# Optimization experiments

Measured on AMD Instinct MI355X. Metric: run time of the kernel, lower is better.

Reference implementation:

```python
import jax, jax.numpy as jnp
import numpy as np

K = 128
HEADS = 8
B = 4
T = 2048


def setup_inputs() -> dict:
    key = jax.random.key(0)
    ks = jax.random.split(key, 6)
    x = jax.random.normal(ks[0], (B, T, K), dtype=jnp.float32)
    s = 1.0 / np.sqrt(K)
    # torch nn.Linear weights are (out_features, in_features)
    Wq = jax.random.uniform(ks[1], (HEADS * K, K), dtype=jnp.float32, minval=-s, maxval=s)
    Wk = jax.random.uniform(ks[2], (HEADS * K, K), dtype=jnp.float32, minval=-s, maxval=s)
    Wv = jax.random.uniform(ks[3], (HEADS * K, K), dtype=jnp.float32, minval=-s, maxval=s)
    su = 1.0 / np.sqrt(HEADS * K)
    Wu = jax.random.uniform(ks[4], (K, HEADS * K), dtype=jnp.float32, minval=-su, maxval=su)
    bu = jax.random.uniform(ks[5], (K,), dtype=jnp.float32, minval=-su, maxval=su)
    return {"x": x, "Wq": Wq, "Wk": Wk, "Wv": Wv, "Wu": Wu, "bu": bu}


def reference(x, Wq, Wk, Wv, Wu, bu):
    b, t, k = x.shape
    h = HEADS
    # project: Linear(k, k*h) then view(b,t,h,k); weight reshaped to (h, k_out, k_in)
    q = jnp.einsum('btk,hdk->bhtd', x, Wq.reshape(h, k, k))
    kk = jnp.einsum('btk,hdk->bhtd', x, Wk.reshape(h, k, k))
    v = jnp.einsum('btk,hdk->bhtd', x, Wv.reshape(h, k, k))
    scale = jnp.asarray(k, x.dtype) ** 0.25
    q = q / scale
    kk = kk / scale
    dot = jnp.einsum('bhtd,bhsd->bhts', q, kk)  # [b,h,t,t]
    att = jax.nn.softmax(dot, axis=-1)
    out = jnp.einsum('bhts,bhsd->bhtd', att, v)  # [b,h,t,k]
    out = out.transpose(0, 2, 1, 3).reshape(b, t, h * k)
    return out @ Wu.T + bu
```

## Files before the change

kernel.cpp:

```cpp
#include <hip/hip_runtime.h>
#include <cmath>

namespace {

constexpr int HEADS = 8;
constexpr int Bn = 4;
constexpr int Tn = 2048;
constexpr int Dn = 128;
constexpr float Q_PRESCALE = 0.1275174340f;

typedef _Float16 half8 __attribute__((ext_vector_type(8)));
typedef _Float16 half4 __attribute__((ext_vector_type(4)));
typedef _Float16 half2v __attribute__((ext_vector_type(2)));
typedef float f32x4 __attribute__((ext_vector_type(4)));
typedef float f32x16 __attribute__((ext_vector_type(16)));
typedef unsigned int u32;
typedef unsigned int u32x4 __attribute__((ext_vector_type(4)));

__global__ __launch_bounds__(256) void cast_kernel(
    const float* __restrict__ x, const float* __restrict__ Wq, const float* __restrict__ Wk,
    const float* __restrict__ Wv, const float* __restrict__ Wu, _Float16* __restrict__ xh,
    _Float16* __restrict__ WH) {
  const int idx = blockIdx.x * 256 + threadIdx.x;
  const size_t base = (size_t)idx * 8;
  const float* src;
  _Float16* dst;
  if (base < 1048576) {
    src = x + base;
    dst = xh + base;
  } else {
    const size_t r = base - 1048576;
    const int s = (int)(r >> 17);
    src = ((s == 0) ? Wq : (s == 1) ? Wk : (s == 2) ? Wv : Wu) + (r & 131071);
    dst = WH + r;
  }
  const float4 a = *reinterpret_cast<const float4*>(src);
  const float4 b = *reinterpret_cast<const float4*>(src + 4);
  half8 h;
  h[0] = (_Float16)a.x; h[1] = (_Float16)a.y; h[2] = (_Float16)a.z; h[3] = (_Float16)a.w;
  h[4] = (_Float16)b.x; h[5] = (_Float16)b.y; h[6] = (_Float16)b.z; h[7] = (_Float16)b.w;
  *reinterpret_cast<half8*>(dst) = h;
}

__global__ __launch_bounds__(256, 4) void proj_kernel(const _Float16* __restrict__ xh,
                                                      const _Float16* __restrict__ WH,
                                                      _Float16* __restrict__ Qh,
                                                      _Float16* __restrict__ Kh,
                                                      _Float16* __restrict__ Vt) {
  __shared__ _Float16 sB[128 * 136];
  const int tid = threadIdx.x;
  const int w = tid >> 6, lane = tid & 63, quad = lane >> 4, l16 = lane & 15;
  const int m0 = blockIdx.x * 128;
  const int n0 = blockIdx.y * 128;

#pragma unroll
  for (int it = 0; it < 8; ++it) {
    const int fid = tid + it * 256;
    const int r = fid >> 4, g = fid & 15;
    const half8 v = *reinterpret_cast<const half8*>(WH + (size_t)(n0 + r) * 128 + g * 8);
    const int p = g ^ (r & 15);
    *reinterpret_cast<half8*>(sB + r * 128 + p * 8) = v;
  }

  half8 af[2][4];
  const _Float16* xp = xh + (size_t)(m0 + w * 32 + l16) * 128 + quad * 8;
#pragma unroll
  for (int mt = 0; mt < 2; ++mt)
#pragma unroll
    for (int kk = 0; kk < 4; ++kk)
      af[mt][kk] = *reinterpret_cast<const half8*>(xp + mt * 16 * 128 + kk * 32);

  __syncthreads();

  f32x4 acc[2][8];
#pragma unroll
  for (int mt = 0; mt < 2; ++mt)
#pragma unroll
    for (int nt = 0; nt < 8; ++nt) acc[mt][nt] = (f32x4){0.f, 0.f, 0.f, 0.f};

#pragma unroll
  for (int kk = 0; kk < 4; ++kk)
#pragma unroll
    for (int nt = 0; nt < 8; ++nt) {
      const int r = nt * 16 + l16;
      const int p = (kk * 4 + quad) ^ l16;
      const half8 bf = *reinterpret_cast<const half8*>(sB + r * 128 + p * 8);
      acc[0][nt] = __builtin_amdgcn_mfma_f32_16x16x32_f16(af[0][kk], bf, acc[0][nt], 0, 0, 0);
      acc[1][nt] = __builtin_amdgcn_mfma_f32_16x16x32_f16(af[1][kk], bf, acc[1][nt], 0, 0, 0);
    }

  const int sel = n0 >> 10;
  const int h = (n0 >> 7) & 7;
  const int b = m0 >> 11;
  const int t0b = m0 & 2047;
  const int bh = b * HEADS + h;
  const float scale = (sel == 0) ? Q_PRESCALE : 1.0f;

  __syncthreads();

  if (sel < 2) {
#pragma unroll
    for (int mt = 0; mt < 2; ++mt)
#pragma unroll
      for (int nt = 0; nt < 8; ++nt)
#pragma unroll
        for (int r = 0; r < 4; ++r)
          sB[(w * 32 + mt * 16 + quad * 4 + r) * 136 + nt * 16 + l16] =
              (_Float16)(acc[mt][nt][r] * scale);
  } else {
#pragma unroll
    for (int mt = 0; mt < 2; ++mt)
#pragma unroll
      for (int nt = 0; nt < 8; ++nt)
#pragma unroll
        for (int r = 0; r < 4; ++r)
          sB[(nt * 16 + l16) * 136 + w * 32 + mt * 16 + quad * 4 + r] = (_Float16)acc[mt][nt][r];
  }
  __syncthreads();

  _Float16* dstbase;
  size_t rstride;
  if (sel == 0) {
    dstbase = Qh + ((size_t)bh * Tn + t0b) * Dn;
    rstride = Dn;
  } else if (sel == 1) {
    dstbase = Kh + ((size_t)bh * Tn + t0b) * Dn;
    rstride = Dn;
  } else {
    dstbase = Vt + ((size_t)bh * Dn) * Tn + t0b;
    rstride = Tn;
  }
#pragma unroll
  for (int it = 0; it < 8; ++it) {
    const int fid = tid + it * 256;
    const int r = fid >> 4, g = fid & 15;
    const half8 v = *reinterpret_cast<const half8*>(sB + r * 136 + g * 8);
    *reinterpret_cast<half8*>(dstbase + (size_t)r * rstride + g * 8) = v;
  }
}

__global__ __launch_bounds__(512, 2) void flash_kernel(const _Float16* __restrict__ Qh,
                                                       const _Float16* __restrict__ Kh,
                                                       const _Float16* __restrict__ Vt,
                                                       _Float16* __restrict__ Obh) {
  __shared__ _Float16 sAll[40960];

  const int tid = threadIdx.x;
  const int w = tid >> 6;
  const int lane = tid & 63;
  const int l31 = lane & 31;
  const int h = lane >> 5;
  const int qt = blockIdx.x;
  const int bh = blockIdx.y;
  constexpr int NT = Tn / 64;

  half8 qf[8];
  {
    const _Float16* Qp = Qh + ((size_t)bh * Tn + qt * 256 + w * 32 + l31) * Dn + h * 8;
#pragma unroll
    for (int ds = 0; ds < 8; ++ds) qf[ds] = *reinterpret_cast<const half8*>(Qp + ds * 16);
  }

  const _Float16* Kp = Kh + (size_t)bh * Tn * Dn;
  const _Float16* Vp = Vt + (size_t)bh * Dn * Tn;

  f32x16 o[4];
#pragma unroll
  for (int db = 0; db < 4; ++db) o[db] = (f32x16)(0.f);
  float lsum = 0.f;

  half8 kreg[2], vreg[2];
  const int kr = tid >> 4, kg = tid & 15;
  const int vr = tid >> 3, vg = tid & 7;
  const int vG = (vg >> 1) * 2;
  const int vO = (vg & 1) * 4;

#pragma unroll
  for (int it = 0; it < 2; ++it) {
    kreg[it] = *reinterpret_cast<const half8*>(Kp + (size_t)(kr + it * 32) * Dn + kg * 8);
    vreg[it] = *reinterpret_cast<const half8*>(Vp + (size_t)(vr + it * 64) * Tn + vg * 8);
  }
  {
    _Float16* sK0 = sAll;
    _Float16* sV0 = sAll + 16384;
#pragma unroll
    for (int it = 0; it < 2; ++it) {
      const int r = kr + it * 32;
      const int p = kg ^ (r & 15);
      *reinterpret_cast<half8*>(sK0 + r * 128 + p * 8) = kreg[it];
      const int rv = vr + it * 64;
      const int sw = (rv & 7) ^ ((rv >> 1) & 4);
      const half8 v = vreg[it];
      half4 lo, hi;
      lo[0] = v[0]; lo[1] = v[1]; lo[2] = v[2]; lo[3] = v[3];
      hi[0] = v[4]; hi[1] = v[5]; hi[2] = v[6]; hi[3] = v[7];
      *reinterpret_cast<half4*>(sV0 + rv * 64 + ((vG ^ sw) * 8) + vO) = lo;
      *reinterpret_cast<half4*>(sV0 + rv * 64 + (((vG + 1) ^ sw) * 8) + vO) = hi;
    }
  }
#pragma unroll
  for (int it = 0; it < 2; ++it) {
    kreg[it] = *reinterpret_cast<const half8*>(Kp + (size_t)(64 + kr + it * 32) * Dn + kg * 8);
    vreg[it] = *reinterpret_cast<const half8*>(Vp + (size_t)(vr + it * 64) * Tn + 64 + vg * 8);
  }
  __syncthreads();

  f32x16 scA[2], scB[2];
  scA[0] = (f32x16)(0.f);
  scA[1] = (f32x16)(0.f);
#pragma unroll
  for (int ds = 0; ds < 8; ++ds) {
    const int p = (ds * 2 + h) ^ (l31 & 15);
    const half8 kf0 = *reinterpret_cast<const half8*>(sAll + l31 * 128 + p * 8);
    const half8 kf1 = *reinterpret_cast<const half8*>(sAll + (32 + l31) * 128 + p * 8);
    scA[0] = __builtin_amdgcn_mfma_f32_32x32x16_f16(kf0, qf[ds], scA[0], 0, 0, 0);
    scA[1] = __builtin_amdgcn_mfma_f32_32x32x16_f16(kf1, qf[ds], scA[1], 0, 0, 0);
  }

  auto step = [&](int t, f32x16 (&sc)[2], f32x16 (&sn)[2]) {
    _Float16* sKn = sAll + ((t + 1) & 1) * 8192;
    _Float16* sVc = sAll + 16384 + (t % 3) * 8192;
    _Float16* sVn = sAll + 16384 + ((t + 1) % 3) * 8192;

    if (t + 1 < NT) {
#pragma unroll
      for (int it = 0; it < 2; ++it) {
        const int r = kr + it * 32;
        const int p = kg ^ (r & 15);
        *reinterpret_cast<half8*>(sKn + r * 128 + p * 8) = kreg[it];
        const int rv = vr + it * 64;
        const int sw = (rv & 7) ^ ((rv >> 1) & 4);
        const half8 v = vreg[it];
        half4 lo, hi;
        lo[0] = v[0]; lo[1] = v[1]; lo[2] = v[2]; lo[3] = v[3];
        hi[0] = v[4]; hi[1] = v[5]; hi[2] = v[6]; hi[3] = v[7];
        *reinterpret_cast<half4*>(sVn + rv * 64 + ((vG ^ sw) * 8) + vO) = lo;
        *reinterpret_cast<half4*>(sVn + rv * 64 + (((vG + 1) ^ sw) * 8) + vO) = hi;
      }
    }
    __syncthreads();
    if (t + 2 < NT) {
      const _Float16* knext = Kp + (size_t)(t + 2) * 64 * Dn;
      const _Float16* vnext = Vp + (t + 2) * 64;
#pragma unroll
      for (int it = 0; it < 2; ++it) {
        kreg[it] = *reinterpret_cast<const half8*>(knext + (size_t)(kr + it * 32) * Dn + kg * 8);
        vreg[it] = *reinterpret_cast<const half8*>(vnext + (size_t)(vr + it * 64) * Tn + vg * 8);
      }
    }

    if (t + 1 < NT) {
      sn[0] = (f32x16)(0.f);
      sn[1] = (f32x16)(0.f);
    }

    half8 bfr[4];
#pragma unroll
    for (int i = 0; i < 2; ++i) {
      const int kb = i;
      {
        u32 pk[8];
        float part = 0.f;
#pragma unroll
        for (int j = 0; j < 8; ++j) {
          const float e0 = __builtin_amdgcn_exp2f(sc[kb][2 * j]);
          const float e1 = __builtin_amdgcn_exp2f(sc[kb][2 * j + 1]);
          part += e0 + e1;
          half2v hp = {(_Float16)e0, (_Float16)e1};
          pk[j] = __builtin_bit_cast(u32, hp);
        }
        lsum += part;
        u32x4 beven = {pk[0], pk[1], pk[2], pk[3]};
        u32x4 bodd = {pk[4], pk[5], pk[6], pk[7]};
        bfr[kb * 2] = __builtin_bit_cast(half8, beven);
        bfr[kb * 2 + 1] = __builtin_bit_cast(half8, bodd);
      }
      if (t + 1 < NT) {
#pragma unroll
        for (int dd = 0; dd < 4; ++dd) {
          const int ds = 4 * i + dd;
          const int p = (ds * 2 + h) ^ (l31 & 15);
          const half8 kf0 = *reinterpret_cast<const half8*>(sKn + l31 * 128 + p * 8);
          const half8 kf1 = *reinterpret_cast<const half8*>(sKn + (32 + l31) * 128 + p * 8);
          sn[0] = __builtin_amdgcn_mfma_f32_32x32x16_f16(kf0, qf[ds], sn[0], 0, 0, 0);
          sn[1] = __builtin_amdgcn_mfma_f32_32x32x16_f16(kf1, qf[ds], sn[1], 0, 0, 0);
        }
      }
      if (i >= 1) {
#pragma unroll
        for (int kk = 0; kk < 2; ++kk) {
          const int kb16 = kk;
#pragma unroll
          for (int db = 0; db < 4; ++db) {
            const int r = db * 32 + l31;
            const int pv = (kb16 * 2 + h) ^ ((r & 7) ^ ((r >> 1) & 4));
            const half8 vf = *reinterpret_cast<const half8*>(sVc + r * 64 + pv * 8);
            o[db] = __builtin_amdgcn_mfma_f32_32x32x16_f16(vf, bfr[kb16], o[db], 0, 0, 0);
          }
        }
      }
    }
#pragma unroll
    for (int kk = 2; kk < 4; ++kk) {
      const int kb16 = kk;
#pragma unroll
      for (int db = 0; db < 4; ++db) {
        const int r = db * 32 + l31;
        const int pv = (kb16 * 2 + h) ^ ((r & 7) ^ ((r >> 1) & 4));
        const half8 vf = *reinterpret_cast<const half8*>(sVc + r * 64 + pv * 8);
        o[db] = __builtin_amdgcn_mfma_f32_32x32x16_f16(vf, bfr[kb16], o[db], 0, 0, 0);
      }
    }
  };

  for (int st = 0; st < NT; st += 2) {
    step(st, scA, scB);
    step(st + 1, scB, scA);
  }

  float inv;
  {
    float ls = lsum;
    ls += __shfl_xor(ls, 32);
    inv = 1.0f / ls;
  }

  __syncthreads();
  _Float16* const sO = sAll + w * 4096;

  {
    const int qrow = l31;
#pragma unroll
    for (int db = 0; db < 4; ++db)
#pragma unroll
      for (int grp = 0; grp < 4; ++grp) {
        const int d0 = db * 32 + grp * 8 + h * 4;
        half4 hv;
#pragma unroll
        for (int i = 0; i < 4; ++i) hv[i] = (_Float16)(o[db][grp * 4 + i] * inv);
        const int idx = qrow * 128 + (((d0 >> 3) ^ (qrow & 15)) << 3) + (d0 & 7);
        *reinterpret_cast<half4*>(sO + idx) = hv;
      }
  }
  const int b = bh >> 3, hh = bh & 7;
#pragma unroll
  for (int it = 0; it < 8; ++it) {
    const int idx = lane + it * 64;
    const int row = idx >> 4, g = idx & 15;
    const half8 v = *reinterpret_cast<const half8*>(sO + row * 128 + ((g ^ (row & 15)) << 3));
    const size_t t = (size_t)(b * Tn + qt * 256 + w * 32 + row);
    *reinterpret_cast<half8*>(Obh + t * (HEADS * Dn) + hh * 128 + g * 8) = v;
  }
}

__global__ __launch_bounds__(256, 2) void outproj_kernel(const _Float16* __restrict__ Obh,
                                                         const _Float16* __restrict__ Wuh,
                                                         const float* __restrict__ bu,
                                                         float* __restrict__ out) {
  __shared__ float sR[4 * 32 * 128];
  const int tid = threadIdx.x;
  const int w = tid >> 6, lane = tid & 63, quad = lane >> 4, l16 = lane & 15;
  const int r0 = blockIdx.x * 32;

  f32x4 acc[2][8];
#pragma unroll
  for (int mt = 0; mt < 2; ++mt)
#pragma unroll
    for (int nt = 0; nt < 8; ++nt) acc[mt][nt] = (f32x4){0.f, 0.f, 0.f, 0.f};

  const _Float16* ap = Obh + (size_t)(r0 + l16) * 1024 + w * 256 + quad * 8;
  const _Float16* bp = Wuh + (size_t)l16 * 1024 + w * 256 + quad * 8;

#pragma unroll
  for (int kk = 0; kk < 8; ++kk) {
    const half8 a0 = *reinterpret_cast<const half8*>(ap + kk * 32);
    const half8 a1 = *reinterpret_cast<const half8*>(ap + 16 * 1024 + kk * 32);
#pragma unroll
    for (int nt = 0; nt < 8; ++nt) {
      const half8 bf = *reinterpret_cast<const half8*>(bp + (size_t)nt * 16 * 1024 + kk * 32);
      acc[0][nt] = __builtin_amdgcn_mfma_f32_16x16x32_f16(a0, bf, acc[0][nt], 0, 0, 0);
      acc[1][nt] = __builtin_amdgcn_mfma_f32_16x16x32_f16(a1, bf, acc[1][nt], 0, 0, 0);
    }
  }

#pragma unroll
  for (int mt = 0; mt < 2; ++mt)
#pragma unroll
    for (int nt = 0; nt < 8; ++nt)
#pragma unroll
      for (int r = 0; r < 4; ++r)
        sR[w * 4096 + (mt * 16 + quad * 4 + r) * 128 + nt * 16 + l16] = acc[mt][nt][r];
  __syncthreads();

#pragma unroll
  for (int it = 0; it < 16; ++it) {
    const int idx = tid + it * 256;
    const int row = idx >> 7, col = idx & 127;
    const float v = sR[idx] + sR[4096 + idx] + sR[8192 + idx] + sR[12288 + idx] + bu[col];
    out[(size_t)(r0 + row) * Dn + col] = v;
  }
}

}

extern "C" void kernel_launch(void* const* d_in, const int* in_sizes, int n_in, void* d_out,
                              int out_size, void* d_ws, size_t ws_size, hipStream_t stream) {
  (void)in_sizes; (void)n_in; (void)out_size; (void)ws_size;
  const float* x = (const float*)d_in[0];
  const float* Wq = (const float*)d_in[1];
  const float* Wk = (const float*)d_in[2];
  const float* Wv = (const float*)d_in[3];
  const float* Wu = (const float*)d_in[4];
  const float* bu = (const float*)d_in[5];
  float* out = (float*)d_out;

  constexpr size_t NE = (size_t)Bn * HEADS * Tn * Dn;
  char* ws = (char*)d_ws;
  _Float16* xh = (_Float16*)ws;
  _Float16* WH = (_Float16*)(ws + 2097152);
  _Float16* Qh = (_Float16*)(ws + 4194304);
  _Float16* Kh = (_Float16*)(ws + 4194304 + NE * 2);
  _Float16* Vt = (_Float16*)(ws + 4194304 + NE * 4);
  _Float16* Obh = (_Float16*)(ws + 4194304 + NE * 6);
  _Float16* Wuh = WH + 393216;

  cast_kernel<<<dim3(768), 256, 0, stream>>>(x, Wq, Wk, Wv, Wu, xh, WH);
  proj_kernel<<<dim3(64, 24), 256, 0, stream>>>(xh, WH, Qh, Kh, Vt);
  flash_kernel<<<dim3(8, 32), 512, 0, stream>>>(Qh, Kh, Vt, Obh);
  outproj_kernel<<<dim3(256), 256, 0, stream>>>(Obh, Wuh, bu, out);
}
```

Measured before the change: 170.1 us.

## Fuse fp32 cast into projections, remap flash blocks per XCD, add MFMA priority

Removes the separate cast kernel: the projection and output-projection kernels now read fp32 inputs and weights and convert them to fp16 in registers. The flash kernel remaps block indices so that blocks sharing a batch-head land on the same XCD, aiming for better L2 reuse of K and V. It also raises wave priority around MFMA sections. The output projection moves to 16-row tiles with more blocks and higher occupancy. This trades one launch and an intermediate buffer for repeated fp32 weight loads and conversions inside each block.

```diff
diff --git a/kernel.cpp b/kernel.cpp
--- a/kernel.cpp
+++ b/kernel.cpp
@@ -17,33 +17,19 @@
 typedef unsigned int u32;
 typedef unsigned int u32x4 __attribute__((ext_vector_type(4)));
 
-__global__ __launch_bounds__(256) void cast_kernel(
-    const float* __restrict__ x, const float* __restrict__ Wq, const float* __restrict__ Wk,
-    const float* __restrict__ Wv, const float* __restrict__ Wu, _Float16* __restrict__ xh,
-    _Float16* __restrict__ WH) {
-  const int idx = blockIdx.x * 256 + threadIdx.x;
-  const size_t base = (size_t)idx * 8;
-  const float* src;
-  _Float16* dst;
-  if (base < 1048576) {
-    src = x + base;
-    dst = xh + base;
-  } else {
-    const size_t r = base - 1048576;
-    const int s = (int)(r >> 17);
-    src = ((s == 0) ? Wq : (s == 1) ? Wk : (s == 2) ? Wv : Wu) + (r & 131071);
-    dst = WH + r;
-  }
-  const float4 a = *reinterpret_cast<const float4*>(src);
-  const float4 b = *reinterpret_cast<const float4*>(src + 4);
+__device__ inline half8 cvt8(const float* p) {
+  const float4 a = *reinterpret_cast<const float4*>(p);
+  const float4 b = *reinterpret_cast<const float4*>(p + 4);
   half8 h;
   h[0] = (_Float16)a.x; h[1] = (_Float16)a.y; h[2] = (_Float16)a.z; h[3] = (_Float16)a.w;
   h[4] = (_Float16)b.x; h[5] = (_Float16)b.y; h[6] = (_Float16)b.z; h[7] = (_Float16)b.w;
-  *reinterpret_cast<half8*>(dst) = h;
-}
-
-__global__ __launch_bounds__(256, 4) void proj_kernel(const _Float16* __restrict__ xh,
-                                                      const _Float16* __restrict__ WH,
+  return h;
+}
+
+__global__ __launch_bounds__(256, 4) void proj_kernel(const float* __restrict__ x,
+                                                      const float* __restrict__ Wq,
+                                                      const float* __restrict__ Wk,
+                                                      const float* __restrict__ Wv,
                                                       _Float16* __restrict__ Qh,
                                                       _Float16* __restrict__ Kh,
                                                       _Float16* __restrict__ Vt) {
@@ -52,23 +38,25 @@
   const int w = tid >> 6, lane = tid & 63, quad = lane >> 4, l16 = lane & 15;
   const int m0 = blockIdx.x * 128;
   const int n0 = blockIdx.y * 128;
+  const int sel = n0 >> 10;
+  const float* Wsel = (sel == 0) ? Wq : (sel == 1) ? Wk : Wv;
+  const int nrow0 = n0 & 1023;
 
 #pragma unroll
   for (int it = 0; it < 8; ++it) {
     const int fid = tid + it * 256;
     const int r = fid >> 4, g = fid & 15;
-    const half8 v = *reinterpret_cast<const half8*>(WH + (size_t)(n0 + r) * 128 + g * 8);
+    const half8 v = cvt8(Wsel + (size_t)(nrow0 + r) * 128 + g * 8);
     const int p = g ^ (r & 15);
     *reinterpret_cast<half8*>(sB + r * 128 + p * 8) = v;
   }
 
   half8 af[2][4];
-  const _Float16* xp = xh + (size_t)(m0 + w * 32 + l16) * 128 + quad * 8;
+  const float* xp = x + (size_t)(m0 + w * 32 + l16) * 128 + quad * 8;
 #pragma unroll
   for (int mt = 0; mt < 2; ++mt)
 #pragma unroll
-    for (int kk = 0; kk < 4; ++kk)
-      af[mt][kk] = *reinterpret_cast<const half8*>(xp + mt * 16 * 128 + kk * 32);
+    for (int kk = 0; kk < 4; ++kk) af[mt][kk] = cvt8(xp + mt * 16 * 128 + kk * 32);
 
   __syncthreads();
 
@@ -89,7 +77,6 @@
       acc[1][nt] = __builtin_amdgcn_mfma_f32_16x16x32_f16(af[1][kk], bf, acc[1][nt], 0, 0, 0);
     }
 
-  const int sel = n0 >> 10;
   const int h = (n0 >> 7) & 7;
   const int b = m0 >> 11;
   const int t0b = m0 & 2047;
@@ -150,8 +137,10 @@
   const int lane = tid & 63;
   const int l31 = lane & 31;
   const int h = lane >> 5;
-  const int qt = blockIdx.x;
-  const int bh = blockIdx.y;
+  const int lid = blockIdx.x + 8 * blockIdx.y;
+  const int xcd = lid & 7, j = lid >> 3;
+  const int bh = xcd * 4 + (j >> 3);
+  const int qt = j & 7;
   constexpr int NT = Tn / 64;
 
   half8 qf[8];
@@ -233,6 +222,7 @@
         const half8 v = vreg[it];
         half4 lo, hi;
         lo[0] = v[0]; lo[1] = v[1]; lo[2] = v[2]; lo[3] = v[3];
+        hi[0] = v[4]; hi[1] = v[5]; hi[2] = v[6]; hi[7 - 7] = v[4];
         hi[0] = v[4]; hi[1] = v[5]; hi[2] = v[6]; hi[3] = v[7];
         *reinterpret_cast<half4*>(sVn + rv * 64 + ((vG ^ sw) * 8) + vO) = lo;
         *reinterpret_cast<half4*>(sVn + rv * 64 + (((vG + 1) ^ sw) * 8) + vO) = hi;
@@ -262,12 +252,12 @@
         u32 pk[8];
         float part = 0.f;
 #pragma unroll
-        for (int j = 0; j < 8; ++j) {
-          const float e0 = __builtin_amdgcn_exp2f(sc[kb][2 * j]);
-          const float e1 = __builtin_amdgcn_exp2f(sc[kb][2 * j + 1]);
+        for (int j2 = 0; j2 < 8; ++j2) {
+          const float e0 = __builtin_amdgcn_exp2f(sc[kb][2 * j2]);
+          const float e1 = __builtin_amdgcn_exp2f(sc[kb][2 * j2 + 1]);
           part += e0 + e1;
           half2v hp = {(_Float16)e0, (_Float16)e1};
-          pk[j] = __builtin_bit_cast(u32, hp);
+          pk[j2] = __builtin_bit_cast(u32, hp);
         }
         lsum += part;
         u32x4 beven = {pk[0], pk[1], pk[2], pk[3]};
@@ -276,6 +266,7 @@
         bfr[kb * 2 + 1] = __builtin_bit_cast(half8, bodd);
       }
       if (t + 1 < NT) {
+        __builtin_amdgcn_s_setprio(1);
 #pragma unroll
         for (int dd = 0; dd < 4; ++dd) {
           const int ds = 4 * i + dd;
@@ -285,8 +276,10 @@
           sn[0] = __builtin_amdgcn_mfma_f32_32x32x16_f16(kf0, qf[ds], sn[0], 0, 0, 0);
           sn[1] = __builtin_amdgcn_mfma_f32_32x32x16_f16(kf1, qf[ds], sn[1], 0, 0, 0);
         }
+        __builtin_amdgcn_s_setprio(0);
       }
       if (i >= 1) {
+        __builtin_amdgcn_s_setprio(1);
 #pragma unroll
         for (int kk = 0; kk < 2; ++kk) {
           const int kb16 = kk;
@@ -298,8 +291,10 @@
             o[db] = __builtin_amdgcn_mfma_f32_32x32x16_f16(vf, bfr[kb16], o[db], 0, 0, 0);
           }
         }
-      }
-    }
+        __builtin_amdgcn_s_setprio(0);
+      }
+    }
+    __builtin_amdgcn_s_setprio(1);
 #pragma unroll
     for (int kk = 2; kk < 4; ++kk) {
       const int kb16 = kk;
@@ -311,6 +306,7 @@
         o[db] = __builtin_amdgcn_mfma_f32_32x32x16_f16(vf, bfr[kb16], o[db], 0, 0, 0);
       }
     }
+    __builtin_amdgcn_s_setprio(0);
   };
 
   for (int st = 0; st < NT; st += 2) {
@@ -353,50 +349,44 @@
   }
 }
 
-__global__ __launch_bounds__(256, 2) void outproj_kernel(const _Float16* __restrict__ Obh,
-                                                         const _Float16* __restrict__ Wuh,
+__global__ __launch_bounds__(256, 4) void outproj_kernel(const _Float16* __restrict__ Obh,
+                                                         const float* __restrict__ Wu,
                                                          const float* __restrict__ bu,
                                                          float* __restrict__ out) {
-  __shared__ float sR[4 * 32 * 128];
+  __shared__ float sR[4 * 16 * 128];
   const int tid = threadIdx.x;
   const int w = tid >> 6, lane = tid & 63, quad = lane >> 4, l16 = lane & 15;
-  const int r0 = blockIdx.x * 32;
-
-  f32x4 acc[2][8];
-#pragma unroll
-  for (int mt = 0; mt < 2; ++mt)
-#pragma unroll
-    for (int nt = 0; nt < 8; ++nt) acc[mt][nt] = (f32x4){0.f, 0.f, 0.f, 0.f};
+  const int r0 = blockIdx.x * 16;
+
+  f32x4 acc[8];
+#pragma unroll
+  for (int nt = 0; nt < 8; ++nt) acc[nt] = (f32x4){0.f, 0.f, 0.f, 0.f};
 
   const _Float16* ap = Obh + (size_t)(r0 + l16) * 1024 + w * 256 + quad * 8;
-  const _Float16* bp = Wuh + (size_t)l16 * 1024 + w * 256 + quad * 8;
+  const float* bp = Wu + (size_t)l16 * 1024 + w * 256 + quad * 8;
 
 #pragma unroll
   for (int kk = 0; kk < 8; ++kk) {
     const half8 a0 = *reinterpret_cast<const half8*>(ap + kk * 32);
-    const half8 a1 = *reinterpret_cast<const half8*>(ap + 16 * 1024 + kk * 32);
 #pragma unroll
     for (int nt = 0; nt < 8; ++nt) {
-      const half8 bf = *reinterpret_cast<const half8*>(bp + (size_t)nt * 16 * 1024 + kk * 32);
-      acc[0][nt] = __builtin_amdgcn_mfma_f32_16x16x32_f16(a0, bf, acc[0][nt], 0, 0, 0);
-      acc[1][nt] = __builtin_amdgcn_mfma_f32_16x16x32_f16(a1, bf, acc[1][nt], 0, 0, 0);
-    }
-  }
-
-#pragma unroll
-  for (int mt = 0; mt < 2; ++mt)
-#pragma unroll
-    for (int nt = 0; nt < 8; ++nt)
-#pragma unroll
-      for (int r = 0; r < 4; ++r)
-        sR[w * 4096 + (mt * 16 + quad * 4 + r) * 128 + nt * 16 + l16] = acc[mt][nt][r];
-  __syncthreads();
-
-#pragma unroll
-  for (int it = 0; it < 16; ++it) {
+      const half8 bf = cvt8(bp + (size_t)nt * 16 * 1024 + kk * 32);
+      acc[nt] = __builtin_amdgcn_mfma_f32_16x16x32_f16(a0, bf, acc[nt], 0, 0, 0);
+    }
+  }
+
+#pragma unroll
+  for (int nt = 0; nt < 8; ++nt)
+#pragma unroll
+    for (int r = 0; r < 4; ++r)
+      sR[w * 2048 + (quad * 4 + r) * 128 + nt * 16 + l16] = acc[nt][r];
+  __syncthreads();
+
+#pragma unroll
+  for (int it = 0; it < 8; ++it) {
     const int idx = tid + it * 256;
     const int row = idx >> 7, col = idx & 127;
-    const float v = sR[idx] + sR[4096 + idx] + sR[8192 + idx] + sR[12288 + idx] + bu[col];
+    const float v = sR[idx] + sR[2048 + idx] + sR[4096 + idx] + sR[6144 + idx] + bu[col];
     out[(size_t)(r0 + row) * Dn + col] = v;
   }
 }
@@ -416,16 +406,12 @@
 
   constexpr size_t NE = (size_t)Bn * HEADS * Tn * Dn;
   char* ws = (char*)d_ws;
-  _Float16* xh = (_Float16*)ws;
-  _Float16* WH = (_Float16*)(ws + 2097152);
-  _Float16* Qh = (_Float16*)(ws + 4194304);
-  _Float16* Kh = (_Float16*)(ws + 4194304 + NE * 2);
-  _Float16* Vt = (_Float16*)(ws + 4194304 + NE * 4);
-  _Float16* Obh = (_Float16*)(ws + 4194304 + NE * 6);
-  _Float16* Wuh = WH + 393216;
-
-  cast_kernel<<<dim3(768), 256, 0, stream>>>(x, Wq, Wk, Wv, Wu, xh, WH);
-  proj_kernel<<<dim3(64, 24), 256, 0, stream>>>(xh, WH, Qh, Kh, Vt);
+  _Float16* Qh = (_Float16*)ws;
+  _Float16* Kh = (_Float16*)(ws + NE * 2);
+  _Float16* Vt = (_Float16*)(ws + NE * 4);
+  _Float16* Obh = (_Float16*)(ws + NE * 6);
+
+  proj_kernel<<<dim3(64, 24), 256, 0, stream>>>(x, Wq, Wk, Wv, Qh, Kh, Vt);
   flash_kernel<<<dim3(8, 32), 512, 0, stream>>>(Qh, Kh, Vt, Obh);
-  outproj_kernel<<<dim3(256), 256, 0, stream>>>(Obh, Wuh, bu, out);
-}
+  outproj_kernel<<<dim3(512), 256, 0, stream>>>(Obh, Wu, bu, out);
+}
```

Result: slower. 188.5 us (+10.8%).
